# Kernel optimization log

Measured on AMD Instinct MI355X. Metric: run time of the kernel, lower is better.

The kernel has to match this reference:

```python
import jax, jax.numpy as jnp
import numpy as np

LENGTH = 2  # pad width per side, from init_kwargs

def setup_inputs() -> dict:
    key = jax.random.key(0)
    x = jax.random.normal(key, (32, 256, 56, 56), dtype=jnp.float32)
    return {"x": x}

def reference(x) -> jnp.ndarray:
    # The torch module is an explicit replicate (edge) pad of width LENGTH on H and W.
    # Corners are filled with the nearest corner pixel, matching jnp.pad mode='edge'.
    return jnp.pad(x, ((0, 0), (0, 0), (LENGTH, LENGTH), (LENGTH, LENGTH)), mode="edge")
```

## Files before the change

### kernel.cpp

```cpp
#include <hip/hip_runtime.h>


#define IN_H  56
#define IN_W  56
#define OUT_H 60
#define OUT_W 60
#define PAD   2
#define W4    (OUT_W / 4)

typedef float f4u __attribute__((ext_vector_type(4), aligned(4)));
typedef float f4a __attribute__((ext_vector_type(4), aligned(16)));

__global__ __launch_bounds__(256) void pad2d_edge_kernel(
    const float* __restrict__ in, float* __restrict__ out, int n_vec) {
    int idx = blockIdx.x * blockDim.x + threadIdx.x;
    if (idx >= n_vec) return;

    int w4 = idx % W4;
    int t  = idx / W4;
    int oh = t % OUT_H;
    int nc = t / OUT_H;

    int ih = min(max(oh - PAD, 0), IN_H - 1);
    const float* src = in + (size_t)nc * (IN_H * IN_W) + (size_t)ih * IN_W;

    int ow0  = w4 * 4;
    int base = min(max(ow0 - PAD, 0), IN_W - 4);
    f4u u = *reinterpret_cast<const f4u*>(src + base);

    f4a v;
    v.x = (w4 == W4 - 1) ? u.z : u.x;
    v.y = (w4 == 0)      ? u.x : ((w4 == W4 - 1) ? u.w : u.y);
    v.z = (w4 == 0)      ? u.x : ((w4 == W4 - 1) ? u.w : u.z);
    v.w = (w4 == 0)      ? u.y : ((w4 == W4 - 1) ? u.w : u.w);

    __builtin_nontemporal_store(v, reinterpret_cast<f4a*>(out) + idx);
}

extern "C" void kernel_launch(void* const* d_in, const int* in_sizes, int n_in,
                              void* d_out, int out_size, void* d_ws, size_t ws_size,
                              hipStream_t stream) {
    const float* x = (const float*)d_in[0];
    float* out = (float*)d_out;

    int n_vec = out_size / 4;
    int block = 256;
    int grid = (n_vec + block - 1) / block;
    pad2d_edge_kernel<<<grid, block, 0, stream>>>(x, out, n_vec);
}
```

Before: 187.9 us.

## Use aligned 16-byte loads with DPP row shift for edge-pad neighbors

```diff
diff --git a/kernel.cpp b/kernel.cpp
--- a/kernel.cpp
+++ b/kernel.cpp
@@ -7,34 +7,45 @@
 #define OUT_W 60
 #define PAD   2
 #define W4    (OUT_W / 4)
+#define LPR   16
 
-typedef float f4u __attribute__((ext_vector_type(4), aligned(4)));
 typedef float f4a __attribute__((ext_vector_type(4), aligned(16)));
 
+__device__ __forceinline__ float dpp_row_shr1(float x) {
+    int xi = __builtin_bit_cast(int, x);
+    int r  = __builtin_amdgcn_update_dpp(xi, xi, 0x111 ,
+                                         0xf , 0xf ,
+                                         false );
+    return __builtin_bit_cast(float, r);
+}
+
 __global__ __launch_bounds__(256) void pad2d_edge_kernel(
-    const float* __restrict__ in, float* __restrict__ out, int n_vec) {
+    const float* __restrict__ in, float* __restrict__ out, int n_thr) {
     int idx = blockIdx.x * blockDim.x + threadIdx.x;
-    if (idx >= n_vec) return;
-
-    int w4 = idx % W4;
-    int t  = idx / W4;
+    if (idx >= n_thr) return;
+    int l = idx & (LPR - 1);
+    int t = idx >> 4;
     int oh = t % OUT_H;
     int nc = t / OUT_H;
 
     int ih = min(max(oh - PAD, 0), IN_H - 1);
-    const float* src = in + (size_t)nc * (IN_H * IN_W) + (size_t)ih * IN_W;
+    const f4a* src = reinterpret_cast<const f4a*>(
+        in + (size_t)nc * (IN_H * IN_W) + (size_t)ih * IN_W);
 
-    int ow0  = w4 * 4;
-    int base = min(max(ow0 - PAD, 0), IN_W - 4);
-    f4u u = *reinterpret_cast<const f4u*>(src + base);
+    f4a u = src[min(l, IN_W / 4 - 1)];
+
+    float a = dpp_row_shr1(u.z);
+    float b = dpp_row_shr1(u.w);
 
     f4a v;
-    v.x = (w4 == W4 - 1) ? u.z : u.x;
-    v.y = (w4 == 0)      ? u.x : ((w4 == W4 - 1) ? u.w : u.y);
-    v.z = (w4 == 0)      ? u.x : ((w4 == W4 - 1) ? u.w : u.z);
-    v.w = (w4 == 0)      ? u.y : ((w4 == W4 - 1) ? u.w : u.w);
+    v.x = (l == 0)      ? u.x : a;
+    v.y = (l == 0)      ? u.x : b;
+    v.z = (l == W4 - 1) ? b   : u.x;
+    v.w = (l == W4 - 1) ? b   : u.y;
 
-    __builtin_nontemporal_store(v, reinterpret_cast<f4a*>(out) + idx);
+    if (l < W4)
+        __builtin_nontemporal_store(
+            v, reinterpret_cast<f4a*>(out) + (size_t)t * W4 + l);
 }
 
 extern "C" void kernel_launch(void* const* d_in, const int* in_sizes, int n_in,
@@ -43,8 +54,9 @@
     const float* x = (const float*)d_in[0];
     float* out = (float*)d_out;
 
-    int n_vec = out_size / 4;
+    int nc_planes = out_size / (OUT_H * OUT_W);
+    int n_thr = nc_planes * OUT_H * LPR;
     int block = 256;
-    int grid = (n_vec + block - 1) / block;
-    pad2d_edge_kernel<<<grid, block, 0, stream>>>(x, out, n_vec);
+    int grid = (n_thr + block - 1) / block;
+    pad2d_edge_kernel<<<grid, block, 0, stream>>>(x, out, n_thr);
 }
```

After: 191.1 us. Within noise of the previous version (+1.7%).
